# Kernel optimization log

Hardware: AMD Instinct MI355X
Metric: run time of the kernel (lower is better)

The kernel has to match this reference:

```python
import jax, jax.numpy as jnp
import numpy as np

N = 30000      # nodes
E = 480000     # edges per etype (avg degree 16)
IN = 256       # in_feats
OUT = 256      # out_feats
H = 4          # num_heads
DH = OUT // H  # per-head dim
K = 16         # fixed neighbor-table degree for top-5 / bottom-2 selection
ETYPES = ("rur", "rsr", "rtr")
NEG_SLOPE = 0.2


def setup_inputs() -> dict:
    key = jax.random.key(0)
    ks = iter(jax.random.split(key, 64))
    d = {"h": jax.random.normal(next(ks), (N, IN), jnp.float32)}
    for et in ETYPES:
        d[f"src_{et}"] = jax.random.randint(next(ks), (E,), 0, N)
        d[f"dst_{et}"] = jax.random.randint(next(ks), (E,), 0, N)
        d[f"ew_{et}"] = jax.random.uniform(next(ks), (E,), jnp.float32)
        d[f"nbr_idx_{et}"] = jax.random.randint(next(ks), (N, K), 0, N)
        d[f"nbr_w_{et}"] = jax.random.uniform(next(ks), (N, K), jnp.float32)
        # GATConv params: fc weight, attention vectors, bias
        d[f"W_{et}"] = jax.random.normal(next(ks), (IN, OUT), jnp.float32) / np.sqrt(IN)
        d[f"al_{et}"] = jax.random.normal(next(ks), (H, DH), jnp.float32) * 0.1
        d[f"ar_{et}"] = jax.random.normal(next(ks), (H, DH), jnp.float32) * 0.1
        d[f"b_{et}"] = jnp.zeros((OUT,), jnp.float32)
    d["Wt"] = jax.random.normal(next(ks), (OUT, 8), jnp.float32) / np.sqrt(OUT)
    d["bt"] = jnp.zeros((8,), jnp.float32)
    d["Wb"] = jax.random.normal(next(ks), (OUT, 8), jnp.float32) / np.sqrt(OUT)
    d["bb"] = jnp.zeros((8,), jnp.float32)
    d["Wp"] = jax.random.normal(next(ks), (OUT + 16, OUT), jnp.float32) / np.sqrt(OUT + 16)
    d["bp"] = jnp.zeros((OUT,), jnp.float32)
    return d


def _gat(h, src, dst, ew, W, al, ar, b):
    # DGL GATConv (eval mode): feat = h@W split into heads; additive attention;
    # edge softmax over destination; post-softmax edge_weight scaling.
    feat = (h @ W).reshape(N, H, DH)                       # [N,H,DH]
    el = (feat * al).sum(-1)                               # [N,H]
    er = (feat * ar).sum(-1)                               # [N,H]
    e = jax.nn.leaky_relu(el[src] + er[dst], NEG_SLOPE)    # [E,H]
    m = jax.ops.segment_max(e, dst, num_segments=N)        # stable softmax per dst
    ex = jnp.exp(e - m[dst])
    a = ex / jax.ops.segment_sum(ex, dst, num_segments=N)[dst]
    a = a * ew[:, None]                                    # edge_weight scaling
    msg = (a[:, :, None] * feat[src]).reshape(E, OUT)      # [E,OUT]
    return jax.ops.segment_sum(msg, dst, num_segments=N) + b


def _enhance(gat_out, nbr_idx, nbr_w, Wt, bt, Wb, bb, Wp, bp):
    # top-5 / bottom-2 neighbors by weight, mean-pooled, small MLPs, projection
    nbr_emb = gat_out[nbr_idx]                                          # [N,K,OUT]
    ti = jax.lax.top_k(nbr_w, 5)[1]                                     # [N,5]
    top5 = jnp.take_along_axis(nbr_emb, ti[:, :, None], axis=1).mean(1)
    bi = jax.lax.top_k(-nbr_w, 2)[1]                                    # [N,2]
    bot2 = jnp.take_along_axis(nbr_emb, bi[:, :, None], axis=1).mean(1)
    t = top5 @ Wt + bt                                                  # [N,8]
    bo = bot2 @ Wb + bb                                                 # [N,8]
    return jnp.concatenate([gat_out, t, bo], axis=-1) @ Wp + bp         # [N,OUT]


def reference(h,
              src_rur, dst_rur, ew_rur, nbr_idx_rur, nbr_w_rur,
              W_rur, al_rur, ar_rur, b_rur,
              src_rsr, dst_rsr, ew_rsr, nbr_idx_rsr, nbr_w_rsr,
              W_rsr, al_rsr, ar_rsr, b_rsr,
              src_rtr, dst_rtr, ew_rtr, nbr_idx_rtr, nbr_w_rtr,
              W_rtr, al_rtr, ar_rtr, b_rtr,
              Wt, bt, Wb, bb, Wp, bp):
    edges = {
        "rur": (src_rur, dst_rur, ew_rur, nbr_idx_rur, nbr_w_rur, W_rur, al_rur, ar_rur, b_rur),
        "rsr": (src_rsr, dst_rsr, ew_rsr, nbr_idx_rsr, nbr_w_rsr, W_rsr, al_rsr, ar_rsr, b_rsr),
        "rtr": (src_rtr, dst_rtr, ew_rtr, nbr_idx_rtr, nbr_w_rtr, W_rtr, al_rtr, ar_rtr, b_rtr),
    }
    outs = []
    for et in ETYPES:
        src, dst, ew, nidx, nw, W, al, ar, b = edges[et]
        g = _gat(h, src, dst, ew, W, al, ar, b)
        outs.append(_enhance(g, nidx, nw, Wt, bt, Wb, bb, Wp, bp))
    return jnp.concatenate(outs, axis=1)  # [N, 3*OUT]
```

## Files before the change

### kernel.cpp

```cpp
#include <hip/hip_runtime.h>
#include <hip/hip_fp16.h>

#define N_NODES 30000
#define N_EDGES 480000
#define NB 64
#define CHUNK 7500

typedef _Float16 f16;
typedef f16 f16x8 __attribute__((ext_vector_type(8)));
typedef float f32x4 __attribute__((ext_vector_type(4)));

__global__ void convert_h_kernel(const float* __restrict__ in, f16* __restrict__ out, int n8)
{
  int i = blockIdx.x * 256 + threadIdx.x;
  if (i >= n8) return;
  float4 a = *(const float4*)(in + (size_t)i * 8);
  float4 b = *(const float4*)(in + (size_t)i * 8 + 4);
  f16x8 v;
  v[0] = (f16)a.x; v[1] = (f16)a.y; v[2] = (f16)a.z; v[3] = (f16)a.w;
  v[4] = (f16)b.x; v[5] = (f16)b.y; v[6] = (f16)b.z; v[7] = (f16)b.w;
  *(f16x8*)(out + (size_t)i * 8) = v;
}

__global__ void transpose_w_kernel(const float* __restrict__ s0, const float* __restrict__ s1,
                                   const float* __restrict__ s2, const float* __restrict__ s3,
                                   f16* __restrict__ out)
{
  int m = blockIdx.y;
  const float* in = (m == 0) ? s0 : (m == 1) ? s1 : (m == 2) ? s2 : s3;
  int t = blockIdx.x * 256 + threadIdx.x;
  int n = t >> 8, k = t & 255;
  out[(size_t)m * 65536 + t] = (f16)in[k * 256 + n];
}

__global__ void w12_kernel(const float* __restrict__ Wp, f16* __restrict__ W12T)
{
  int t = blockIdx.x * 256 + threadIdx.x;
  if (t >= 256 * 40) return;
  int col = t / 40, k = t % 40;
  f16 v = (f16)0.f;
  if (k < 8)       v = (f16)Wp[(size_t)(256 + k) * 256 + col];
  else if (k < 16) v = (f16)Wp[(size_t)(264 + (k - 8)) * 256 + col];
  W12T[t] = v;
}

__global__ void w16_kernel(const float* __restrict__ Wt, const float* __restrict__ Wb,
                           f16* __restrict__ W16T)
{
  int t = blockIdx.x * 256 + threadIdx.x;
  if (t >= 16 * 256) return;
  int j = t >> 8, k = t & 255;
  W16T[t] = (f16)((j < 8) ? Wt[(size_t)k * 8 + j] : Wb[(size_t)k * 8 + (j - 8)]);
}

template<int MODE>
__global__ __launch_bounds__(512)
void gemm_mfma(const f16* __restrict__ A, const f16* __restrict__ BT,
               f16* __restrict__ Ch, float* __restrict__ Cf, int M,
               const float* __restrict__ al, const float* __restrict__ ar,
               float* __restrict__ el, float* __restrict__ er,
               const float* __restrict__ tvec, const float* __restrict__ bvec,
               const f16* __restrict__ W12Tg, const float* __restrict__ bp,
               int ldc, int coff)
{
  __shared__ alignas(16) f16 Bs[256][264];
  __shared__ alignas(16) f16 W12s[MODE ? 256 : 1][MODE ? 40 : 8];

  const int tid = threadIdx.x;
  const int lane = tid & 63, wv = tid >> 6;
  const int l15 = lane & 15, lq = lane >> 4;
  const int wr = wv >> 1, wc = wv & 1;
  const int bm = blockIdx.x * 128;
  const int cb = wc * 128;

#pragma unroll
  for (int i = 0; i < 16; ++i) {
    int seg = tid + i * 512;
    int row = seg >> 5;
    int cs = (seg & 31) * 8;
    *(uint4*)&Bs[row][cs] = *(const uint4*)&BT[(size_t)row * 256 + cs];
  }
  if (MODE == 1) {
    for (int i = tid; i < 2560; i += 512)
      ((uint2*)&W12s[0][0])[i] = ((const uint2*)W12Tg)[i];
  }
  __syncthreads();

  const int r0 = bm + wr * 32 + l15;
  const int r1 = r0 + 16;
  const bool ok0 = r0 < M, ok1 = r1 < M;
  const f16* Arow0 = A + (size_t)r0 * 256;
  const f16* Arow1 = A + (size_t)r1 * 256;

  f32x4 acc[2][8] = {};

#pragma unroll
  for (int k0 = 0; k0 < 256; k0 += 32) {
    int ko = k0 + lq * 8;
    f16x8 a0 = {0, 0, 0, 0, 0, 0, 0, 0};
    f16x8 a1 = {0, 0, 0, 0, 0, 0, 0, 0};
    if (ok0) a0 = *(const f16x8*)(Arow0 + ko);
    if (ok1) a1 = *(const f16x8*)(Arow1 + ko);
#pragma unroll
    for (int nf = 0; nf < 8; ++nf) {
      f16x8 bf = *(const f16x8*)&Bs[cb + nf * 16 + l15][ko];
      acc[0][nf] = __builtin_amdgcn_mfma_f32_16x16x32_f16(a0, bf, acc[0][nf], 0, 0, 0);
      acc[1][nf] = __builtin_amdgcn_mfma_f32_16x16x32_f16(a1, bf, acc[1][nf], 0, 0, 0);
    }
  }

  if (MODE == 0) {
    float alv[8], arv[8];
#pragma unroll
    for (int nf = 0; nf < 8; ++nf) {
      alv[nf] = al[cb + nf * 16 + l15];
      arv[nf] = ar[cb + nf * 16 + l15];
    }
#pragma unroll
    for (int m = 0; m < 2; ++m)
#pragma unroll
      for (int i = 0; i < 4; ++i) {
        int row = bm + wr * 32 + m * 16 + lq * 4 + i;
        float peA = 0.f, prA = 0.f, peB = 0.f, prB = 0.f;
#pragma unroll
        for (int nf = 0; nf < 4; ++nf) {
          peA = fmaf(acc[m][nf][i], alv[nf], peA);
          prA = fmaf(acc[m][nf][i], arv[nf], prA);
          peB = fmaf(acc[m][nf + 4][i], alv[nf + 4], peB);
          prB = fmaf(acc[m][nf + 4][i], arv[nf + 4], prB);
        }
#pragma unroll
        for (int o = 8; o >= 1; o >>= 1) {
          peA += __shfl_xor(peA, o, 64);
          prA += __shfl_xor(prA, o, 64);
          peB += __shfl_xor(peB, o, 64);
          prB += __shfl_xor(prB, o, 64);
        }
        if (row < M) {
          if (l15 == 0) {
            int hA = wc * 2;
            el[row * 4 + hA] = peA;     er[row * 4 + hA] = prA;
            el[row * 4 + hA + 1] = peB; er[row * 4 + hA + 1] = prB;
          }
#pragma unroll
          for (int nf = 0; nf < 8; ++nf)
            Ch[(size_t)row * 256 + cb + nf * 16 + l15] = (f16)acc[m][nf][i];
        }
      }
  } else {
#pragma unroll
    for (int m = 0; m < 2; ++m) {
      int arow = bm + wr * 32 + m * 16 + l15;
      f16x8 af = {0, 0, 0, 0, 0, 0, 0, 0};
      if (arow < M && lq < 2) {
        const float* srcp = (lq == 0) ? &tvec[(size_t)arow * 8] : &bvec[(size_t)arow * 8];
        float4 x0 = *(const float4*)srcp;
        float4 x1 = *(const float4*)(srcp + 4);
        af[0] = (f16)x0.x; af[1] = (f16)x0.y; af[2] = (f16)x0.z; af[3] = (f16)x0.w;
        af[4] = (f16)x1.x; af[5] = (f16)x1.y; af[6] = (f16)x1.z; af[7] = (f16)x1.w;
      }
#pragma unroll
      for (int nf = 0; nf < 8; ++nf) {
        f16x8 bf2 = *(const f16x8*)&W12s[cb + nf * 16 + l15][lq * 8];
        acc[m][nf] = __builtin_amdgcn_mfma_f32_16x16x32_f16(af, bf2, acc[m][nf], 0, 0, 0);
      }
    }
    float bpv[8];
#pragma unroll
    for (int nf = 0; nf < 8; ++nf) bpv[nf] = bp[cb + nf * 16 + l15];
#pragma unroll
    for (int m = 0; m < 2; ++m)
#pragma unroll
      for (int i = 0; i < 4; ++i) {
        int row = bm + wr * 32 + m * 16 + lq * 4 + i;
        if (row >= M) continue;
#pragma unroll
        for (int nf = 0; nf < 8; ++nf)
          Cf[(size_t)row * ldc + coff + cb + nf * 16 + l15] = acc[m][nf][i] + bpv[nf];
      }
  }
}

__global__ __launch_bounds__(512)
void hist_kernel(const int* __restrict__ d0, const int* __restrict__ d1,
                 const int* __restrict__ d2, unsigned short* __restrict__ ghist,
                 unsigned short* __restrict__ rank16)
{
  __shared__ unsigned int h32[N_NODES / 2];
  int et = blockIdx.y, b = blockIdx.x, tid = threadIdx.x;
  const int* dst = (et == 0) ? d0 : (et == 1) ? d1 : d2;
  for (int i = tid; i < N_NODES / 2; i += 512) h32[i] = 0u;
  __syncthreads();
  int e0 = b * CHUNK;
  for (int i = tid; i < CHUNK; i += 512) {
    int e = e0 + i;
    int d = dst[e];
    unsigned int sh = (d & 1) * 16;
    unsigned int old = atomicAdd(&h32[d >> 1], 1u << sh);
    rank16[(size_t)et * N_EDGES + e] = (unsigned short)((old >> sh) & 0xFFFFu);
  }
  __syncthreads();
  unsigned short* gh = ghist + ((size_t)(et * NB + b)) * N_NODES;
  for (int d = tid; d < N_NODES; d += 512)
    gh[d] = (unsigned short)((h32[d >> 1] >> ((d & 1) * 16)) & 0xFFFFu);
}

__global__ __launch_bounds__(256)
void blockpfx_kernel(unsigned short* __restrict__ ghist, int* __restrict__ counts)
{
  int d = blockIdx.x * 256 + threadIdx.x;
  int et = blockIdx.y;
  if (d >= N_NODES) return;
  int running = 0;
#pragma unroll
  for (int b = 0; b < NB; ++b) {
    size_t idx = ((size_t)(et * NB + b)) * N_NODES + d;
    int v = ghist[idx];
    ghist[idx] = (unsigned short)running;
    running += v;
  }
  counts[et * N_NODES + d] = running;
}

__global__ __launch_bounds__(1024)
void scan_kernel(int* __restrict__ cc_all, int* __restrict__ off_all, int n, int total)
{
  int et = blockIdx.x;
  int* cc = cc_all + (size_t)et * n;
  int* off = off_all + (size_t)et * (n + 1);
  __shared__ int wsum[16];
  __shared__ int woff[16];
  __shared__ int s_carry, s_chunk;
  int tid = threadIdx.x;
  int lane = tid & 63, wid = tid >> 6;
  if (tid == 0) s_carry = 0;
  __syncthreads();
  for (int base = 0; base < n; base += 1024) {
    int i = base + tid;
    int v = (i < n) ? cc[i] : 0;
    int x = v;
#pragma unroll
    for (int s = 1; s < 64; s <<= 1) {
      int y = __shfl_up(x, s, 64);
      if (lane >= s) x += y;
    }
    if (lane == 63) wsum[wid] = x;
    __syncthreads();
    if (wid == 0 && lane < 16) {
      int ws_ = wsum[lane];
      int xx = ws_;
#pragma unroll
      for (int s = 1; s < 16; s <<= 1) {
        int y = __shfl_up(xx, s, 64);
        if (lane >= s) xx += y;
      }
      woff[lane] = xx - ws_;
      if (lane == 15) s_chunk = xx;
    }
    __syncthreads();
    int excl = s_carry + woff[wid] + (x - v);
    if (i < n) { off[i] = excl; cc[i] = excl; }
    __syncthreads();
    if (tid == 0) s_carry += s_chunk;
    __syncthreads();
  }
  if (tid == 0) off[n] = total;
}

__global__ __launch_bounds__(256)
void place_kernel(const int* __restrict__ d0, const int* __restrict__ d1,
                  const int* __restrict__ d2,
                  const int* __restrict__ s0, const int* __restrict__ s1,
                  const int* __restrict__ s2,
                  const float* __restrict__ w0, const float* __restrict__ w1,
                  const float* __restrict__ w2,
                  const int* __restrict__ off, const unsigned short* __restrict__ ghist,
                  const unsigned short* __restrict__ rank16,
                  unsigned int* __restrict__ csr_pay)
{
  int e = blockIdx.x * 256 + threadIdx.x;
  if (e >= N_EDGES) return;
  int et = blockIdx.y;
  const int* dst = (et == 0) ? d0 : (et == 1) ? d1 : d2;
  const int* src = (et == 0) ? s0 : (et == 1) ? s1 : s2;
  const float* ew = (et == 0) ? w0 : (et == 1) ? w1 : w2;
  int d = dst[e];
  int b = e / CHUNK;
  int pos = off[et * (N_NODES + 1) + d]
          + (int)ghist[((size_t)(et * NB + b)) * N_NODES + d]
          + (int)rank16[(size_t)et * N_EDGES + e];
  unsigned short hw = __half_as_ushort(__float2half_rn(ew[e]));
  csr_pay[(size_t)et * N_EDGES + pos] = (unsigned int)src[e] | ((unsigned int)hw << 16);
}

__global__ __launch_bounds__(512)
void aggregate_kernel(const int* __restrict__ off, const unsigned int* __restrict__ csr_pay,
                      const float* __restrict__ el, const float* __restrict__ er,
                      const __half* __restrict__ feat, const float* __restrict__ bias,
                      __half* __restrict__ gat, int n_nodes)
{
  int tid = threadIdx.x;
  int lane = tid & 63, wv = tid >> 6;
  int lg = lane >> 4, lc = lane & 15;
  int cp = blockIdx.y;
  int n = blockIdx.x * 32 + wv * 4 + lg;
  if (n >= n_nodes) return;
  int cbase = cp * 64 + lc * 4;

  int e0 = off[n], e1 = off[n + 1];
  float ern = er[(size_t)n * 4 + cp];
  float ac0 = 0.f, ac1 = 0.f, ac2 = 0.f, ac3 = 0.f, dn = 0.f;

  int e = e0;
  for (; e + 3 < e1; e += 4) {
    unsigned int p0 = csr_pay[e], p1 = csr_pay[e + 1];
    unsigned int p2 = csr_pay[e + 2], p3 = csr_pay[e + 3];
    int s0 = (int)(p0 & 0xFFFFu), s1 = (int)(p1 & 0xFFFFu);
    int s2 = (int)(p2 & 0xFFFFu), s3 = (int)(p3 & 0xFFFFu);
    float v0 = el[s0 * 4 + cp] + ern; v0 = v0 > 0.f ? v0 : 0.2f * v0;
    float v1 = el[s1 * 4 + cp] + ern; v1 = v1 > 0.f ? v1 : 0.2f * v1;
    float v2 = el[s2 * 4 + cp] + ern; v2 = v2 > 0.f ? v2 : 0.2f * v2;
    float v3 = el[s3 * 4 + cp] + ern; v3 = v3 > 0.f ? v3 : 0.2f * v3;
    float x0 = __expf(v0), x1 = __expf(v1), x2 = __expf(v2), x3 = __expf(v3);
    dn += x0 + x1 + x2 + x3;
    float c0 = x0 * __half2float(__ushort_as_half((unsigned short)(p0 >> 16)));
    float c1 = x1 * __half2float(__ushort_as_half((unsigned short)(p1 >> 16)));
    float c2 = x2 * __half2float(__ushort_as_half((unsigned short)(p2 >> 16)));
    float c3 = x3 * __half2float(__ushort_as_half((unsigned short)(p3 >> 16)));
    uint2 u0 = *(const uint2*)(feat + (size_t)s0 * 256 + cbase);
    uint2 u1 = *(const uint2*)(feat + (size_t)s1 * 256 + cbase);
    uint2 u2 = *(const uint2*)(feat + (size_t)s2 * 256 + cbase);
    uint2 u3 = *(const uint2*)(feat + (size_t)s3 * 256 + cbase);
    float2 A01 = __half22float2(*(__half2*)&u0.x), A23 = __half22float2(*(__half2*)&u0.y);
    float2 B01 = __half22float2(*(__half2*)&u1.x), B23 = __half22float2(*(__half2*)&u1.y);
    float2 C01 = __half22float2(*(__half2*)&u2.x), C23 = __half22float2(*(__half2*)&u2.y);
    float2 D01 = __half22float2(*(__half2*)&u3.x), D23 = __half22float2(*(__half2*)&u3.y);
    ac0 = fmaf(c0, A01.x, ac0); ac1 = fmaf(c0, A01.y, ac1);
    ac2 = fmaf(c0, A23.x, ac2); ac3 = fmaf(c0, A23.y, ac3);
    ac0 = fmaf(c1, B01.x, ac0); ac1 = fmaf(c1, B01.y, ac1);
    ac2 = fmaf(c1, B23.x, ac2); ac3 = fmaf(c1, B23.y, ac3);
    ac0 = fmaf(c2, C01.x, ac0); ac1 = fmaf(c2, C01.y, ac1);
    ac2 = fmaf(c2, C23.x, ac2); ac3 = fmaf(c2, C23.y, ac3);
    ac0 = fmaf(c3, D01.x, ac0); ac1 = fmaf(c3, D01.y, ac1);
    ac2 = fmaf(c3, D23.x, ac2); ac3 = fmaf(c3, D23.y, ac3);
  }
  for (; e < e1; ++e) {
    unsigned int p0 = csr_pay[e];
    int s0 = (int)(p0 & 0xFFFFu);
    float v0 = el[s0 * 4 + cp] + ern; v0 = v0 > 0.f ? v0 : 0.2f * v0;
    float x0 = __expf(v0);
    dn += x0;
    float c0 = x0 * __half2float(__ushort_as_half((unsigned short)(p0 >> 16)));
    uint2 u0 = *(const uint2*)(feat + (size_t)s0 * 256 + cbase);
    float2 A01 = __half22float2(*(__half2*)&u0.x), A23 = __half22float2(*(__half2*)&u0.y);
    ac0 = fmaf(c0, A01.x, ac0); ac1 = fmaf(c0, A01.y, ac1);
    ac2 = fmaf(c0, A23.x, ac2); ac3 = fmaf(c0, A23.y, ac3);
  }

  float invd = (dn != 0.f) ? 1.f / dn : 0.f;
  float4 bv = *(const float4*)&bias[cbase];
  __half2 h01 = __floats2half2_rn(ac0 * invd + bv.x, ac1 * invd + bv.y);
  __half2 h23 = __floats2half2_rn(ac2 * invd + bv.z, ac3 * invd + bv.w);
  uint2 st;
  st.x = *(unsigned int*)&h01;
  st.y = *(unsigned int*)&h23;
  *(uint2*)&gat[(size_t)n * 256 + cbase] = st;
}

__global__ __launch_bounds__(256)
void project_mfma_kernel(const f16* __restrict__ gat, const f16* __restrict__ W16T,
                         float* __restrict__ gt, float* __restrict__ gb, int M)
{
  __shared__ alignas(16) f16 Ws[16][256];
  int tid = threadIdx.x;
  for (int i = tid; i < 512; i += 256)
    ((uint4*)&Ws[0][0])[i] = ((const uint4*)W16T)[i];
  __syncthreads();

  int lane = tid & 63, wv = tid >> 6;
  int l15 = lane & 15, lq = lane >> 4;
  int bm = blockIdx.x * 128 + wv * 32;
  int r0 = bm + l15, r1 = r0 + 16;
  bool ok0 = r0 < M, ok1 = r1 < M;

  f32x4 acc[2] = {};
#pragma unroll
  for (int k0 = 0; k0 < 256; k0 += 32) {
    int ko = k0 + lq * 8;
    f16x8 a0 = {0, 0, 0, 0, 0, 0, 0, 0};
    f16x8 a1 = {0, 0, 0, 0, 0, 0, 0, 0};
    if (ok0) a0 = *(const f16x8*)(gat + (size_t)r0 * 256 + ko);
    if (ok1) a1 = *(const f16x8*)(gat + (size_t)r1 * 256 + ko);
    f16x8 bf = *(const f16x8*)&Ws[l15][ko];
    acc[0] = __builtin_amdgcn_mfma_f32_16x16x32_f16(a0, bf, acc[0], 0, 0, 0);
    acc[1] = __builtin_amdgcn_mfma_f32_16x16x32_f16(a1, bf, acc[1], 0, 0, 0);
  }
#pragma unroll
  for (int m = 0; m < 2; ++m)
#pragma unroll
    for (int i = 0; i < 4; ++i) {
      int row = bm + m * 16 + lq * 4 + i;
      if (row >= M) continue;
      float v = acc[m][i];
      if (l15 < 8) gt[(size_t)row * 8 + l15] = v;
      else         gb[(size_t)row * 8 + (l15 - 8)] = v;
    }
}

__global__ __launch_bounds__(256)
void enhance_pool_kernel(const int* __restrict__ nbr_idx, const float* __restrict__ nbr_w,
                         const float* __restrict__ gt, const float* __restrict__ gb,
                         const float* __restrict__ bt, const float* __restrict__ bb,
                         float* __restrict__ tvec, float* __restrict__ bvec, int n_nodes)
{
  int n = (blockIdx.x * 256 + threadIdx.x) >> 6;
  int lane = threadIdx.x & 63;
  if (n >= n_nodes) return;
  const int l16 = lane & 15;

  float w = nbr_w[(size_t)n * 16 + l16];
  int idx = nbr_idx[(size_t)n * 16 + l16];

  int rhi = 0, rlo = 0;
#pragma unroll
  for (int i = 0; i < 16; ++i) {
    float wi = __shfl(w, i, 64);
    rhi += (wi > w) || (wi == w && i < l16);
    rlo += (wi < w) || (wi == w && i < l16);
  }

  int rows[7];
#pragma unroll
  for (int q = 0; q < 5; ++q) {
    unsigned long long m = __ballot(lane < 16 && rhi == q);
    rows[q] = __shfl(idx, __ffsll(m) - 1, 64);
  }
#pragma unroll
  for (int q = 0; q < 2; ++q) {
    unsigned long long m = __ballot(lane < 16 && rlo == q);
    rows[5 + q] = __shfl(idx, __ffsll(m) - 1, 64);
  }

  int j = lane & 7;
  if (lane < 8) {
    float s = 0.f;
#pragma unroll
    for (int q = 0; q < 5; ++q) s += gt[(size_t)rows[q] * 8 + j];
    tvec[(size_t)n * 8 + j] = s * 0.2f + bt[j];
  } else if (lane < 16) {
    float s = gb[(size_t)rows[5] * 8 + j] + gb[(size_t)rows[6] * 8 + j];
    bvec[(size_t)n * 8 + j] = s * 0.5f + bb[j];
  }
}

extern "C" void kernel_launch(void* const* d_in, const int* in_sizes, int n_in,
                              void* d_out, int out_size, void* d_ws, size_t ws_size,
                              hipStream_t stream)
{
  const int N_ = N_NODES;
  const int E_ = N_EDGES;

  const float* h = (const float*)d_in[0];
  const float* Wt = (const float*)d_in[28];
  const float* bt = (const float*)d_in[29];
  const float* Wb = (const float*)d_in[30];
  const float* bb = (const float*)d_in[31];
  const float* Wp = (const float*)d_in[32];
  const float* bp = (const float*)d_in[33];
  float* out = (float*)d_out;

  char* wsb = (char*)d_ws;
  size_t o = 0;
  auto alloc = [&](size_t bytes) -> void* {
    void* p = wsb + o;
    o = (o + bytes + 255) & ~(size_t)255;
    return p;
  };
  f16*  hf    = (f16*)alloc((size_t)N_ * 256 * 2);
  f16*  feat  = (f16*)alloc((size_t)N_ * 256 * 2);
  f16*  gat   = (f16*)alloc((size_t)N_ * 256 * 2);
  f16*  WT    = (f16*)alloc((size_t)4 * 256 * 256 * 2);
  f16*  W12T  = (f16*)alloc((size_t)256 * 40 * 2);
  f16*  W16T  = (f16*)alloc((size_t)16 * 256 * 2);
  float* el     = (float*)alloc((size_t)N_ * 4 * 4);
  float* er     = (float*)alloc((size_t)N_ * 4 * 4);
  float* gt     = (float*)alloc((size_t)N_ * 8 * 4);
  float* gb     = (float*)alloc((size_t)N_ * 8 * 4);
  float* tvec   = (float*)alloc((size_t)N_ * 8 * 4);
  float* bvec   = (float*)alloc((size_t)N_ * 8 * 4);
  int*   off    = (int*)alloc((size_t)3 * (N_ + 1) * 4);
  int*   counts = (int*)alloc((size_t)3 * N_ * 4);
  unsigned short* ghist = (unsigned short*)alloc((size_t)3 * NB * N_ * 2);
  unsigned short* rank16 = (unsigned short*)alloc((size_t)3 * E_ * 2);
  unsigned int* csr_pay = (unsigned int*)alloc((size_t)3 * E_ * 4);
  (void)ws_size; (void)in_sizes; (void)n_in; (void)out_size;

  const int row_blocks = (N_ + 127) / 128;
  const int edge_blocks = (E_ + 255) / 256;
  const int wave_blocks = (N_ + 3) / 4;
  const int agg_blocks = (N_ + 31) / 32;

  const int* d_dst0 = (const int*)d_in[1 + 0 * 9 + 1];
  const int* d_dst1 = (const int*)d_in[1 + 1 * 9 + 1];
  const int* d_dst2 = (const int*)d_in[1 + 2 * 9 + 1];
  const int* d_src0 = (const int*)d_in[1 + 0 * 9 + 0];
  const int* d_src1 = (const int*)d_in[1 + 1 * 9 + 0];
  const int* d_src2 = (const int*)d_in[1 + 2 * 9 + 0];
  const float* d_ew0 = (const float*)d_in[1 + 0 * 9 + 2];
  const float* d_ew1 = (const float*)d_in[1 + 1 * 9 + 2];
  const float* d_ew2 = (const float*)d_in[1 + 2 * 9 + 2];

  convert_h_kernel<<<(N_ * 256 / 8 + 255) / 256, 256, 0, stream>>>(h, hf, N_ * 256 / 8);
  transpose_w_kernel<<<dim3(256, 4), 256, 0, stream>>>(
      (const float*)d_in[1 + 0 * 9 + 5], (const float*)d_in[1 + 1 * 9 + 5],
      (const float*)d_in[1 + 2 * 9 + 5], Wp, WT);
  w12_kernel<<<(256 * 40 + 255) / 256, 256, 0, stream>>>(Wp, W12T);
  w16_kernel<<<16, 256, 0, stream>>>(Wt, Wb, W16T);
  f16* WpT = WT + (size_t)3 * 65536;

  hist_kernel<<<dim3(NB, 3), 512, 0, stream>>>(d_dst0, d_dst1, d_dst2, ghist, rank16);
  blockpfx_kernel<<<dim3((N_ + 255) / 256, 3), 256, 0, stream>>>(ghist, counts);
  scan_kernel<<<3, 1024, 0, stream>>>(counts, off, N_, E_);
  place_kernel<<<dim3(edge_blocks, 3), 256, 0, stream>>>(
      d_dst0, d_dst1, d_dst2, d_src0, d_src1, d_src2, d_ew0, d_ew1, d_ew2,
      off, ghist, rank16, csr_pay);

  for (int et = 0; et < 3; ++et) {
    const int base = 1 + et * 9;
    const int* nbr_idx = (const int*)d_in[base + 3];
    const float* nbr_w = (const float*)d_in[base + 4];
    const float* al = (const float*)d_in[base + 6];
    const float* ar = (const float*)d_in[base + 7];
    const float* b = (const float*)d_in[base + 8];

    gemm_mfma<0><<<row_blocks, 512, 0, stream>>>(
        hf, WT + (size_t)et * 65536, feat, nullptr, N_, al, ar, el, er,
        nullptr, nullptr, nullptr, nullptr, 256, 0);

    aggregate_kernel<<<dim3(agg_blocks, 4), 512, 0, stream>>>(
        off + (size_t)et * (N_ + 1), csr_pay + (size_t)et * E_,
        el, er, (const __half*)feat, b, (__half*)gat, N_);

    project_mfma_kernel<<<row_blocks, 256, 0, stream>>>(
        gat, W16T, gt, gb, N_);

    enhance_pool_kernel<<<wave_blocks, 256, 0, stream>>>(
        nbr_idx, nbr_w, gt, gb, bt, bb, tvec, bvec, N_);

    gemm_mfma<1><<<row_blocks, 512, 0, stream>>>(
        gat, WpT, nullptr, out, N_, nullptr, nullptr, nullptr, nullptr,
        tvec, bvec, W12T, bp, 768, et * 256);
  }
}
```

Measured before the change: 354.6 us.

## Batch all three edge types into single kernel launches via grid dimension

Replaces the per-edge-type loop of five kernels with one launch per stage that covers all three edge types through an extra grid dimension, using triple-sized intermediate buffers. Per-type attention vectors and biases are packed into contiguous arrays by a new small kernel. The aim is to cut launch count and fill the GPU better, since each per-type launch has only about 235 row blocks. The cost is three times the intermediate memory and a larger working set that may fit cache less well.

```diff
diff --git a/kernel.cpp b/kernel.cpp
--- a/kernel.cpp
+++ b/kernel.cpp
@@ -53,25 +53,47 @@
   W16T[t] = (f16)((j < 8) ? Wt[(size_t)k * 8 + j] : Wb[(size_t)k * 8 + (j - 8)]);
 }
 
+__global__ void pack_params_kernel(const float* __restrict__ al0, const float* __restrict__ al1,
+                                   const float* __restrict__ al2,
+                                   const float* __restrict__ ar0, const float* __restrict__ ar1,
+                                   const float* __restrict__ ar2,
+                                   const float* __restrict__ b0, const float* __restrict__ b1,
+                                   const float* __restrict__ b2,
+                                   float* __restrict__ al_all, float* __restrict__ ar_all,
+                                   float* __restrict__ b_all)
+{
+  int et = blockIdx.x, t = threadIdx.x;
+  const float* al = (et == 0) ? al0 : (et == 1) ? al1 : al2;
+  const float* ar = (et == 0) ? ar0 : (et == 1) ? ar1 : ar2;
+  const float* b  = (et == 0) ? b0 : (et == 1) ? b1 : b2;
+  al_all[et * 256 + t] = al[t];
+  ar_all[et * 256 + t] = ar[t];
+  b_all[et * 256 + t]  = b[t];
+}
+
 template<int MODE>
 __global__ __launch_bounds__(512)
-void gemm_mfma(const f16* __restrict__ A, const f16* __restrict__ BT,
-               f16* __restrict__ Ch, float* __restrict__ Cf, int M,
-               const float* __restrict__ al, const float* __restrict__ ar,
-               float* __restrict__ el, float* __restrict__ er,
-               const float* __restrict__ tvec, const float* __restrict__ bvec,
+void gemm_mfma(const f16* __restrict__ Abase, const f16* __restrict__ BTbase,
+               f16* __restrict__ Chbase, float* __restrict__ Cf, int M,
+               const float* __restrict__ al_all, const float* __restrict__ ar_all,
+               float* __restrict__ el_all, float* __restrict__ er_all,
+               const float* __restrict__ tvec_all, const float* __restrict__ bvec_all,
                const f16* __restrict__ W12Tg, const float* __restrict__ bp,
-               int ldc, int coff)
+               int ldc)
 {
   __shared__ alignas(16) f16 Bs[256][264];
   __shared__ alignas(16) f16 W12s[MODE ? 256 : 1][MODE ? 40 : 8];
 
   const int tid = threadIdx.x;
+  const int et = blockIdx.y;
   const int lane = tid & 63, wv = tid >> 6;
   const int l15 = lane & 15, lq = lane >> 4;
   const int wr = wv >> 1, wc = wv & 1;
   const int bm = blockIdx.x * 128;
   const int cb = wc * 128;
+
+  const f16* A = (MODE == 0) ? Abase : (Abase + (size_t)et * M * 256);
+  const f16* BT = (MODE == 0) ? (BTbase + (size_t)et * 65536) : BTbase;
 
 #pragma unroll
   for (int i = 0; i < 16; ++i) {
@@ -110,6 +132,11 @@
   }
 
   if (MODE == 0) {
+    f16* Ch = Chbase + (size_t)et * M * 256;
+    float* el = el_all + (size_t)et * M * 4;
+    float* er = er_all + (size_t)et * M * 4;
+    const float* al = al_all + et * 256;
+    const float* ar = ar_all + et * 256;
     float alv[8], arv[8];
 #pragma unroll
     for (int nf = 0; nf < 8; ++nf) {
@@ -148,6 +175,9 @@
         }
       }
   } else {
+    const float* tvec = tvec_all + (size_t)et * M * 8;
+    const float* bvec = bvec_all + (size_t)et * M * 8;
+    const int coff = et * 256;
 #pragma unroll
     for (int m = 0; m < 2; ++m) {
       int arow = bm + wr * 32 + m * 16 + l15;
@@ -294,21 +324,28 @@
 }
 
 __global__ __launch_bounds__(512)
-void aggregate_kernel(const int* __restrict__ off, const unsigned int* __restrict__ csr_pay,
-                      const float* __restrict__ el, const float* __restrict__ er,
-                      const __half* __restrict__ feat, const float* __restrict__ bias,
-                      __half* __restrict__ gat, int n_nodes)
+void aggregate_kernel(const int* __restrict__ off_all, const unsigned int* __restrict__ pay_all,
+                      const float* __restrict__ el_all, const float* __restrict__ er_all,
+                      const __half* __restrict__ feat_all, const float* __restrict__ b_all,
+                      __half* __restrict__ gat_all, int n_nodes)
 {
   int tid = threadIdx.x;
   int lane = tid & 63, wv = tid >> 6;
   int lg = lane >> 4, lc = lane & 15;
   int cp = blockIdx.y;
+  int et = blockIdx.z;
   int n = blockIdx.x * 32 + wv * 4 + lg;
   if (n >= n_nodes) return;
   int cbase = cp * 64 + lc * 4;
 
+  const int* off = off_all + (size_t)et * (n_nodes + 1);
+  const unsigned int* csr_pay = pay_all + (size_t)et * N_EDGES;
+  const float* el = el_all + (size_t)et * n_nodes * 4;
+  const __half* feat = feat_all + (size_t)et * n_nodes * 256;
+  const float* bias = b_all + et * 256;
+
   int e0 = off[n], e1 = off[n + 1];
-  float ern = er[(size_t)n * 4 + cp];
+  float ern = er_all[((size_t)et * n_nodes + n) * 4 + cp];
   float ac0 = 0.f, ac1 = 0.f, ac2 = 0.f, ac3 = 0.f, dn = 0.f;
 
   int e = e0;
@@ -364,7 +401,7 @@
   uint2 st;
   st.x = *(unsigned int*)&h01;
   st.y = *(unsigned int*)&h23;
-  *(uint2*)&gat[(size_t)n * 256 + cbase] = st;
+  *(uint2*)&gat_all[((size_t)et * n_nodes + n) * 256 + cbase] = st;
 }
 
 __global__ __launch_bounds__(256)
@@ -408,14 +445,24 @@
 }
 
 __global__ __launch_bounds__(256)
-void enhance_pool_kernel(const int* __restrict__ nbr_idx, const float* __restrict__ nbr_w,
-                         const float* __restrict__ gt, const float* __restrict__ gb,
+void enhance_pool_kernel(const int* __restrict__ ni0, const int* __restrict__ ni1,
+                         const int* __restrict__ ni2,
+                         const float* __restrict__ nw0, const float* __restrict__ nw1,
+                         const float* __restrict__ nw2,
+                         const float* __restrict__ gt_all, const float* __restrict__ gb_all,
                          const float* __restrict__ bt, const float* __restrict__ bb,
-                         float* __restrict__ tvec, float* __restrict__ bvec, int n_nodes)
+                         float* __restrict__ tvec_all, float* __restrict__ bvec_all, int n_nodes)
 {
   int n = (blockIdx.x * 256 + threadIdx.x) >> 6;
   int lane = threadIdx.x & 63;
   if (n >= n_nodes) return;
+  int et = blockIdx.y;
+  const int* nbr_idx = (et == 0) ? ni0 : (et == 1) ? ni1 : ni2;
+  const float* nbr_w = (et == 0) ? nw0 : (et == 1) ? nw1 : nw2;
+  const float* gt = gt_all + (size_t)et * n_nodes * 8;
+  const float* gb = gb_all + (size_t)et * n_nodes * 8;
+  float* tvec = tvec_all + (size_t)et * n_nodes * 8;
+  float* bvec = bvec_all + (size_t)et * n_nodes * 8;
   const int l16 = lane & 15;
 
   float w = nbr_w[(size_t)n * 16 + l16];
@@ -477,17 +524,20 @@
     return p;
   };
   f16*  hf    = (f16*)alloc((size_t)N_ * 256 * 2);
-  f16*  feat  = (f16*)alloc((size_t)N_ * 256 * 2);
-  f16*  gat   = (f16*)alloc((size_t)N_ * 256 * 2);
+  f16*  feat  = (f16*)alloc((size_t)3 * N_ * 256 * 2);
+  f16*  gat   = (f16*)alloc((size_t)3 * N_ * 256 * 2);
   f16*  WT    = (f16*)alloc((size_t)4 * 256 * 256 * 2);
   f16*  W12T  = (f16*)alloc((size_t)256 * 40 * 2);
   f16*  W16T  = (f16*)alloc((size_t)16 * 256 * 2);
-  float* el     = (float*)alloc((size_t)N_ * 4 * 4);
-  float* er     = (float*)alloc((size_t)N_ * 4 * 4);
-  float* gt     = (float*)alloc((size_t)N_ * 8 * 4);
-  float* gb     = (float*)alloc((size_t)N_ * 8 * 4);
-  float* tvec   = (float*)alloc((size_t)N_ * 8 * 4);
-  float* bvec   = (float*)alloc((size_t)N_ * 8 * 4);
+  float* al_all = (float*)alloc((size_t)3 * 256 * 4);
+  float* ar_all = (float*)alloc((size_t)3 * 256 * 4);
+  float* b_all  = (float*)alloc((size_t)3 * 256 * 4);
+  float* el     = (float*)alloc((size_t)3 * N_ * 4 * 4);
+  float* er     = (float*)alloc((size_t)3 * N_ * 4 * 4);
+  float* gt     = (float*)alloc((size_t)3 * N_ * 8 * 4);
+  float* gb     = (float*)alloc((size_t)3 * N_ * 8 * 4);
+  float* tvec   = (float*)alloc((size_t)3 * N_ * 8 * 4);
+  float* bvec   = (float*)alloc((size_t)3 * N_ * 8 * 4);
   int*   off    = (int*)alloc((size_t)3 * (N_ + 1) * 4);
   int*   counts = (int*)alloc((size_t)3 * N_ * 4);
   unsigned short* ghist = (unsigned short*)alloc((size_t)3 * NB * N_ * 2);
@@ -499,6 +549,7 @@
   const int edge_blocks = (E_ + 255) / 256;
   const int wave_blocks = (N_ + 3) / 4;
   const int agg_blocks = (N_ + 31) / 32;
+  const int prj_blocks = (3 * N_ + 127) / 128;
 
   const int* d_dst0 = (const int*)d_in[1 + 0 * 9 + 1];
   const int* d_dst1 = (const int*)d_in[1 + 1 * 9 + 1];
@@ -516,6 +567,14 @@
       (const float*)d_in[1 + 2 * 9 + 5], Wp, WT);
   w12_kernel<<<(256 * 40 + 255) / 256, 256, 0, stream>>>(Wp, W12T);
   w16_kernel<<<16, 256, 0, stream>>>(Wt, Wb, W16T);
+  pack_params_kernel<<<3, 256, 0, stream>>>(
+      (const float*)d_in[1 + 0 * 9 + 6], (const float*)d_in[1 + 1 * 9 + 6],
+      (const float*)d_in[1 + 2 * 9 + 6],
+      (const float*)d_in[1 + 0 * 9 + 7], (const float*)d_in[1 + 1 * 9 + 7],
+      (const float*)d_in[1 + 2 * 9 + 7],
+      (const float*)d_in[1 + 0 * 9 + 8], (const float*)d_in[1 + 1 * 9 + 8],
+      (const float*)d_in[1 + 2 * 9 + 8],
+      al_all, ar_all, b_all);
   f16* WpT = WT + (size_t)3 * 65536;
 
   hist_kernel<<<dim3(NB, 3), 512, 0, stream>>>(d_dst0, d_dst1, d_dst2, ghist, rank16);
@@ -525,30 +584,24 @@
       d_dst0, d_dst1, d_dst2, d_src0, d_src1, d_src2, d_ew0, d_ew1, d_ew2,
       off, ghist, rank16, csr_pay);
 
-  for (int et = 0; et < 3; ++et) {
-    const int base = 1 + et * 9;
-    const int* nbr_idx = (const int*)d_in[base + 3];
-    const float* nbr_w = (const float*)d_in[base + 4];
-    const float* al = (const float*)d_in[base + 6];
-    const float* ar = (const float*)d_in[base + 7];
-    const float* b = (const float*)d_in[base + 8];
-
-    gemm_mfma<0><<<row_blocks, 512, 0, stream>>>(
-        hf, WT + (size_t)et * 65536, feat, nullptr, N_, al, ar, el, er,
-        nullptr, nullptr, nullptr, nullptr, 256, 0);
-
-    aggregate_kernel<<<dim3(agg_blocks, 4), 512, 0, stream>>>(
-        off + (size_t)et * (N_ + 1), csr_pay + (size_t)et * E_,
-        el, er, (const __half*)feat, b, (__half*)gat, N_);
-
-    project_mfma_kernel<<<row_blocks, 256, 0, stream>>>(
-        gat, W16T, gt, gb, N_);
-
-    enhance_pool_kernel<<<wave_blocks, 256, 0, stream>>>(
-        nbr_idx, nbr_w, gt, gb, bt, bb, tvec, bvec, N_);
-
-    gemm_mfma<1><<<row_blocks, 512, 0, stream>>>(
-        gat, WpT, nullptr, out, N_, nullptr, nullptr, nullptr, nullptr,
-        tvec, bvec, W12T, bp, 768, et * 256);
-  }
-}
+  gemm_mfma<0><<<dim3(row_blocks, 3), 512, 0, stream>>>(
+      hf, WT, feat, nullptr, N_, al_all, ar_all, el, er,
+      nullptr, nullptr, nullptr, nullptr, 256);
+
+  aggregate_kernel<<<dim3(agg_blocks, 4, 3), 512, 0, stream>>>(
+      off, csr_pay, el, er, (const __half*)feat, b_all, (__half*)gat, N_);
+
+  project_mfma_kernel<<<prj_blocks, 256, 0, stream>>>(
+      gat, W16T, gt, gb, 3 * N_);
+
+  enhance_pool_kernel<<<dim3(wave_blocks, 3), 256, 0, stream>>>(
+      (const int*)d_in[1 + 0 * 9 + 3], (const int*)d_in[1 + 1 * 9 + 3],
+      (const int*)d_in[1 + 2 * 9 + 3],
+      (const float*)d_in[1 + 0 * 9 + 4], (const float*)d_in[1 + 1 * 9 + 4],
+      (const float*)d_in[1 + 2 * 9 + 4],
+      gt, gb, bt, bb, tvec, bvec, N_);
+
+  gemm_mfma<1><<<dim3(row_blocks, 3), 512, 0, stream>>>(
+      gat, WpT, nullptr, out, N_, nullptr, nullptr, nullptr, nullptr,
+      tvec, bvec, W12T, bp, 768);
+}
```

Result: faster. 338.8 us (-4.5%).
